# Kernel tuning notes

Measured on AMD Instinct MI355X. Metric: run time of the kernel, lower is better.

## Reference

```python
import jax, jax.numpy as jnp
import numpy as np
from jax import lax

B, GRID = 256, 58  # 28*2+2 per scn.InputLayer spatial size


def _conv(x, w):
    # x: [B,C,H,W], w: [O,C,k,k]; scn.Convolution is VALID, stride 1, no bias
    return lax.conv_general_dilated(
        x, w, window_strides=(1, 1), padding='VALID',
        dimension_numbers=('NCHW', 'OIHW', 'NCHW'))


def _maxpool2(x):
    return lax.reduce_window(x, -jnp.inf, lax.max,
                             window_dimensions=(1, 1, 2, 2),
                             window_strides=(1, 1, 2, 2), padding='VALID')


def setup_inputs() -> dict:
    key = jax.random.key(0)
    k0, k1, k2, k3, k4 = jax.random.split(key, 5)
    return {
        'x': jax.random.normal(k0, (B, 1, GRID, GRID), dtype=jnp.float32),
        'w1': jax.random.normal(k1, (64, 1, 5, 5), dtype=jnp.float32) * 0.1,
        'w2': jax.random.normal(k2, (128, 64, 5, 5), dtype=jnp.float32) * 0.025,
        'lw': jax.random.normal(k3, (10, 128), dtype=jnp.float32) * 0.09,
        'lb': jax.random.normal(k4, (10,), dtype=jnp.float32) * 0.01,
    }


def reference(x, w1, w2, lw, lb):
    h = _conv(x, w1)          # [B,64,54,54]
    h = _maxpool2(h)          # [B,64,27,27]
    h = _conv(h, w2)          # [B,128,23,23]
    h = jnp.transpose(h, (0, 2, 3, 1))  # channels-last for linear
    return jnp.einsum('bhwc,oc->bhwo', h, lw) + lb  # [B,23,23,10]
```

## Files before the change

kernel.cpp:

```cpp
#include <hip/hip_runtime.h>


typedef __attribute__((ext_vector_type(8))) short bf16x8;
typedef __attribute__((ext_vector_type(4))) float f32x4;
typedef __attribute__((ext_vector_type(16))) float f32x16;
typedef __attribute__((ext_vector_type(2))) unsigned int u32x2;
typedef __attribute__((ext_vector_type(4))) unsigned int u32x4;

#define MFMA16(a, b, c) __builtin_amdgcn_mfma_f32_16x16x32_bf16((a), (b), (c), 0, 0, 0)
#define MFMA32(a, b, c) __builtin_amdgcn_mfma_f32_32x32x16_bf16((a), (b), (c), 0, 0, 0)

static __device__ __forceinline__ unsigned short f2bf(float f) {
    unsigned u = __builtin_bit_cast(unsigned, f);
    u += 0x7FFFu + ((u >> 16) & 1u);
    return (unsigned short)(u >> 16);
}

__global__ __launch_bounds__(256) void prep_w2d(
    const float* __restrict__ w2, unsigned short* __restrict__ w2d)
{
    int t = blockIdx.x * 256 + threadIdx.x;
    if (t >= 25600) return;
    const int lane = t & 63, nt = (t >> 6) & 3, ks = (t >> 8) & 3, kk = t >> 10;
    const int oc = nt * 32 + (lane & 31);
    const int ic0 = ks * 16 + (lane >> 5) * 8;
    unsigned pk[4];
#pragma unroll
    for (int h = 0; h < 4; ++h) {
        unsigned short lo = f2bf(w2[oc * 1600 + (ic0 + 2 * h) * 25 + kk]);
        unsigned short hi = f2bf(w2[oc * 1600 + (ic0 + 2 * h + 1) * 25 + kk]);
        pk[h] = (unsigned)lo | ((unsigned)hi << 16);
    }
    u32x4 v; v.x = pk[0]; v.y = pk[1]; v.z = pk[2]; v.w = pk[3];
    *(u32x4*)(w2d + (size_t)t * 8) = v;
}

#define XS_STR   136
#define XBF_OFF  99144
#define W1T_OFF  105872
#define ECON_STR 272
#define LWT_OFF  147968
#define LDS_TOT  152320

__global__ __launch_bounds__(512, 2) void fused_net(
    const float* __restrict__ x, const float* __restrict__ w1,
    const unsigned short* __restrict__ w2d,
    const float* __restrict__ lw, const float* __restrict__ lb,
    float* __restrict__ out)
{
    extern __shared__ char lds[];
    unsigned short* xbf = (unsigned short*)(lds + XBF_OFF);
    unsigned short* w1t = (unsigned short*)(lds + W1T_OFF);
    const int b = blockIdx.x, tid = threadIdx.x;
    const int lane = tid & 63, w = tid >> 6;
    const int l16 = lane & 15, kg = lane >> 4;
    const int l32 = lane & 31, kg2 = lane >> 5;
    const int mgrp = w >> 1, ngrp = w & 1;

    const float4* xg = (const float4*)(x + b * 3364);
    for (int i = tid; i < 841; i += 512) {
        float4 v = xg[i];
        unsigned p0 = (unsigned)f2bf(v.x) | ((unsigned)f2bf(v.y) << 16);
        unsigned p1 = (unsigned)f2bf(v.z) | ((unsigned)f2bf(v.w) << 16);
        *(uint2*)(xbf + i * 4) = make_uint2(p0, p1);
    }
    for (int i = tid; i < 2048; i += 512) {
        int k = i >> 6, oc = i & 63;
        w1t[i] = (k < 25) ? f2bf(w1[oc * 25 + k]) : (unsigned short)0;
    }
    for (int i = tid; i < 2048; i += 512) {
        int o = i >> 7, cc = i & 127;
        float v = (o < 10) ? lw[o * 128 + cc] : 0.f;
        *(unsigned short*)(lds + LWT_OFF + o * 272 + cc * 2) = f2bf(v);
    }
    __syncthreads();

    {
        int koff[8];
        unsigned kmsk[8];
#pragma unroll
        for (int j = 0; j < 8; ++j) {
            int k = kg * 8 + j;
            int kh = k / 5, kw = k - 5 * kh;
            koff[j] = (k < 25) ? (kh * 58 + kw) : 0;
            kmsk[j] = (k < 25) ? 0xFFFFu : 0u;
        }
        bf16x8 bfrag[4];
#pragma unroll
        for (int ot = 0; ot < 4; ++ot)
#pragma unroll
            for (int j = 0; j < 8; ++j)
                bfrag[ot][j] = (short)w1t[(kg * 8 + j) * 64 + ot * 16 + l16];

        const f32x4 zero4 = {0.f, 0.f, 0.f, 0.f};
        for (int t = w; t < 183; t += 8) {
            int p = t * 4 + (l16 >> 2);
            if (p > 728) p = 728;
            const int q = l16 & 3;
            const int ph = p / 27, pw = p - 27 * ph;
            const int base = (2 * ph + (q >> 1)) * 58 + 2 * pw + (q & 1);
            bf16x8 afrag;
#pragma unroll
            for (int j = 0; j < 8; ++j)
                afrag[j] = (short)(xbf[base + koff[j]] & kmsk[j]);
            f32x4 acc1[4];
#pragma unroll
            for (int ot = 0; ot < 4; ++ot)
                acc1[ot] = MFMA16(afrag, bfrag[ot], zero4);
            const int pout = t * 4 + kg;
            if (pout < 729) {
#pragma unroll
                for (int ot = 0; ot < 4; ++ot) {
                    float m = fmaxf(fmaxf(acc1[ot][0], acc1[ot][1]),
                                    fmaxf(acc1[ot][2], acc1[ot][3]));
                    *(unsigned short*)(lds + pout * XS_STR + (ot * 16 + l16) * 2)
                        = f2bf(m);
                }
            }
        }
    }
    __syncthreads();

    const int mcnt = (mgrp == 0) ? 5 : 4;
    int ts[5], abase[5];
#pragma unroll
    for (int i = 0; i < 5; ++i) {
        int tile = (mgrp == 0) ? i : 5 + (mgrp - 1) * 4 + i;
        if (i >= mcnt) tile = mgrp;
        int tstart = tile * 32;
        if (tstart > 497) tstart = 497;
        ts[i] = tstart;
        const int sp = tstart + l32;
        const int oh = sp / 23, ow = sp - oh * 23;
        abase[i] = (oh * 27 + ow) * XS_STR + kg2 * 16;
    }

    f32x16 acc[5][2];
#pragma unroll
    for (int i = 0; i < 5; ++i)
#pragma unroll
        for (int j = 0; j < 2; ++j)
#pragma unroll
            for (int r = 0; r < 16; ++r) acc[i][j][r] = 0.f;

    for (int kk = 0; kk < 25; ++kk) {
        const int kh = kk / 5, kw = kk - 5 * kh;
        const int pixoff = (kh * 27 + kw) * XS_STR;
        bf16x8 Bf[4][2];
#pragma unroll
        for (int ks = 0; ks < 4; ++ks)
#pragma unroll
            for (int j = 0; j < 2; ++j)
                Bf[ks][j] = *(const bf16x8*)(
                    w2d + ((size_t)kk * 1024 + ks * 256 +
                           (ngrp * 2 + j) * 64 + lane) * 8);
#pragma unroll
        for (int ks = 0; ks < 4; ++ks) {
#pragma unroll
            for (int i = 0; i < 5; ++i) {
                if (i < mcnt) {
                    const char* ap = lds + abase[i] + pixoff + ks * 32;
                    u32x2 lo = *(const u32x2*)(ap);
                    u32x2 hi = *(const u32x2*)(ap + 8);
                    u32x4 t4; t4.x = lo.x; t4.y = lo.y; t4.z = hi.x; t4.w = hi.y;
                    bf16x8 a = __builtin_bit_cast(bf16x8, t4);
                    acc[i][0] = MFMA32(a, Bf[ks][0], acc[i][0]);
                    acc[i][1] = MFMA32(a, Bf[ks][1], acc[i][1]);
                }
            }
        }
    }

    __syncthreads();
#pragma unroll
    for (int i = 0; i < 5; ++i) {
        if (i < mcnt) {
#pragma unroll
            for (int j = 0; j < 2; ++j) {
                const int col = (ngrp * 2 + j) * 32 + l32;
#pragma unroll
                for (int reg = 0; reg < 16; ++reg) {
                    const int row = (reg & 3) + 8 * (reg >> 2) + 4 * kg2;
                    *(unsigned short*)(lds + (ts[i] + row) * ECON_STR + col * 2)
                        = f2bf(acc[i][j][reg]);
                }
            }
        }
    }
    __syncthreads();

    const float lbv = (l16 < 10) ? lb[l16] : 0.f;
#pragma unroll
    for (int i = 0; i < 5; ++i) {
        const int t = w + 8 * i;
        if (t < 34) {
            f32x4 al = {0.f, 0.f, 0.f, 0.f};
            const char* arow = lds + (t * 16 + l16) * ECON_STR + kg * 16;
            const char* brow = lds + LWT_OFF + l16 * 272 + kg * 16;
#pragma unroll
            for (int ks = 0; ks < 4; ++ks) {
                bf16x8 av = *(const bf16x8*)(arow + ks * 64);
                bf16x8 bv = *(const bf16x8*)(brow + ks * 64);
                al = MFMA16(av, bv, al);
            }
            if (l16 < 10) {
#pragma unroll
                for (int r = 0; r < 4; ++r) {
                    int sp = t * 16 + kg * 4 + r;
                    if (sp < 529)
                        out[((size_t)b * 529 + sp) * 10 + l16] = al[r] + lbv;
                }
            }
        }
    }
}

extern "C" void kernel_launch(void* const* d_in, const int* in_sizes, int n_in,
                              void* d_out, int out_size, void* d_ws, size_t ws_size,
                              hipStream_t stream) {
    const float* x  = (const float*)d_in[0];
    const float* w1 = (const float*)d_in[1];
    const float* w2 = (const float*)d_in[2];
    const float* lw = (const float*)d_in[3];
    const float* lb = (const float*)d_in[4];
    float* out = (float*)d_out;

    unsigned short* w2d = (unsigned short*)d_ws;

    (void)hipFuncSetAttribute((const void*)fused_net,
                              hipFuncAttributeMaxDynamicSharedMemorySize,
                              LDS_TOT);

    prep_w2d<<<100, 256, 0, stream>>>(w2, w2d);
    fused_net<<<256, 512, LDS_TOT, stream>>>(x, w1, w2d, lw, lb, out);
}
```

Baseline: 71.75 us.

## Split each image into two row halves per block to double grid parallelism

Each image is now handled by two blocks, each covering about half of the output rows. Each block computes conv1 and pooling only for the input rows its half needs, which cuts LDS to roughly half and raises launch bounds to 4 blocks per CU. The epilogue now stages each tile into a small per-wave-group buffer, and w2 fragments are loaded per k-step to lower register pressure. The cost is recomputing the overlapping halo rows of conv1 in both blocks and adding extra barriers in the epilogue.

```diff
diff --git a/kernel.cpp b/kernel.cpp
--- a/kernel.cpp
+++ b/kernel.cpp
@@ -36,13 +36,14 @@
 }
 
 #define XS_STR   136
-#define XBF_OFF  99144
-#define W1T_OFF  105872
+#define XBF_OFF  62424
+#define W1T_OFF  66832
+#define LWT_OFF  70928
 #define ECON_STR 272
-#define LWT_OFF  147968
-#define LDS_TOT  152320
-
-__global__ __launch_bounds__(512, 2) void fused_net(
+#define ECON_TILE 8704
+#define LDS_TOT  75280
+
+__global__ __launch_bounds__(512, 4) void fused_net(
     const float* __restrict__ x, const float* __restrict__ w1,
     const unsigned short* __restrict__ w2d,
     const float* __restrict__ lw, const float* __restrict__ lb,
@@ -51,18 +52,23 @@
     extern __shared__ char lds[];
     unsigned short* xbf = (unsigned short*)(lds + XBF_OFF);
     unsigned short* w1t = (unsigned short*)(lds + W1T_OFF);
-    const int b = blockIdx.x, tid = threadIdx.x;
+    const int h = blockIdx.x, b = blockIdx.y, tid = threadIdx.x;
     const int lane = tid & 63, w = tid >> 6;
     const int l16 = lane & 15, kg = lane >> 4;
     const int l32 = lane & 31, kg2 = lane >> 5;
     const int mgrp = w >> 1, ngrp = w & 1;
 
-    const float4* xg = (const float4*)(x + b * 3364);
-    for (int i = tid; i < 841; i += 512) {
-        float4 v = xg[i];
-        unsigned p0 = (unsigned)f2bf(v.x) | ((unsigned)f2bf(v.y) << 16);
-        unsigned p1 = (unsigned)f2bf(v.z) | ((unsigned)f2bf(v.w) << 16);
-        *(uint2*)(xbf + i * 4) = make_uint2(p0, p1);
+    const int ph0   = h ? 12 : 0;
+    const int x0    = h ? 24 : 0;
+    const int nxrow = h ? 34 : 38;
+    const int npx   = h ? 405 : 459;
+
+    const float* xb = x + b * 3364 + x0 * 58;
+    const int nf2 = nxrow * 29;
+    for (int i = tid; i < nf2; i += 512) {
+        float2 v = ((const float2*)xb)[i];
+        *(unsigned*)(xbf + i * 2) =
+            (unsigned)f2bf(v.x) | ((unsigned)f2bf(v.y) << 16);
     }
     for (int i = tid; i < 2048; i += 512) {
         int k = i >> 6, oc = i & 63;
@@ -71,7 +77,7 @@
     for (int i = tid; i < 2048; i += 512) {
         int o = i >> 7, cc = i & 127;
         float v = (o < 10) ? lw[o * 128 + cc] : 0.f;
-        *(unsigned short*)(lds + LWT_OFF + o * 272 + cc * 2) = f2bf(v);
+        *(unsigned short*)(lds + LWT_OFF + o * ECON_STR + cc * 2) = f2bf(v);
     }
     __syncthreads();
 
@@ -93,12 +99,14 @@
                 bfrag[ot][j] = (short)w1t[(kg * 8 + j) * 64 + ot * 16 + l16];
 
         const f32x4 zero4 = {0.f, 0.f, 0.f, 0.f};
-        for (int t = w; t < 183; t += 8) {
-            int p = t * 4 + (l16 >> 2);
-            if (p > 728) p = 728;
+        const int nt4 = (npx + 3) >> 2;
+        for (int t = w; t < nt4; t += 8) {
+            int pl = t * 4 + (l16 >> 2);
+            if (pl >= npx) pl = npx - 1;
             const int q = l16 & 3;
-            const int ph = p / 27, pw = p - 27 * ph;
-            const int base = (2 * ph + (q >> 1)) * 58 + 2 * pw + (q & 1);
+            const int pg = ph0 * 27 + pl;
+            const int ph = pg / 27, pw = pg - 27 * ph;
+            const int base = (2 * (ph - ph0) + (q >> 1)) * 58 + 2 * pw + (q & 1);
             bf16x8 afrag;
 #pragma unroll
             for (int j = 0; j < 8; ++j)
@@ -108,7 +116,7 @@
             for (int ot = 0; ot < 4; ++ot)
                 acc1[ot] = MFMA16(afrag, bfrag[ot], zero4);
             const int pout = t * 4 + kg;
-            if (pout < 729) {
+            if (pout < npx) {
 #pragma unroll
                 for (int ot = 0; ot < 4; ++ot) {
                     float m = fmaxf(fmaxf(acc1[ot][0], acc1[ot][1]),
@@ -121,23 +129,27 @@
     }
     __syncthreads();
 
-    const int mcnt = (mgrp == 0) ? 5 : 4;
-    int ts[5], abase[5];
-#pragma unroll
-    for (int i = 0; i < 5; ++i) {
-        int tile = (mgrp == 0) ? i : 5 + (mgrp - 1) * 4 + i;
-        if (i >= mcnt) tile = mgrp;
-        int tstart = tile * 32;
-        if (tstart > 497) tstart = 497;
-        ts[i] = tstart;
-        const int sp = tstart + l32;
+    int ts[3], mcnt;
+    if (h == 0) {
+        if (mgrp == 0) { mcnt = 3; ts[0] = 0; ts[1] = 32; ts[2] = 64; }
+        else { mcnt = 2; ts[0] = 96 + (mgrp - 1) * 64; ts[1] = ts[0] + 32;
+               ts[2] = ts[0]; }
+    } else {
+        mcnt = 2; ts[0] = 288 + mgrp * 64;
+        ts[1] = (mgrp == 3) ? 497 : ts[0] + 32;
+        ts[2] = ts[0];
+    }
+    int abase[3];
+#pragma unroll
+    for (int i = 0; i < 3; ++i) {
+        const int sp = ts[i] + l32;
         const int oh = sp / 23, ow = sp - oh * 23;
-        abase[i] = (oh * 27 + ow) * XS_STR + kg2 * 16;
-    }
-
-    f32x16 acc[5][2];
-#pragma unroll
-    for (int i = 0; i < 5; ++i)
+        abase[i] = ((oh - ph0) * 27 + ow) * XS_STR + kg2 * 16;
+    }
+
+    f32x16 acc[3][2];
+#pragma unroll
+    for (int i = 0; i < 3; ++i)
 #pragma unroll
         for (int j = 0; j < 2; ++j)
 #pragma unroll
@@ -146,73 +158,69 @@
     for (int kk = 0; kk < 25; ++kk) {
         const int kh = kk / 5, kw = kk - 5 * kh;
         const int pixoff = (kh * 27 + kw) * XS_STR;
-        bf16x8 Bf[4][2];
-#pragma unroll
-        for (int ks = 0; ks < 4; ++ks)
-#pragma unroll
-            for (int j = 0; j < 2; ++j)
-                Bf[ks][j] = *(const bf16x8*)(
-                    w2d + ((size_t)kk * 1024 + ks * 256 +
-                           (ngrp * 2 + j) * 64 + lane) * 8);
+        const unsigned short* wp = w2d + ((size_t)kk * 1024 + lane) * 8;
 #pragma unroll
         for (int ks = 0; ks < 4; ++ks) {
-#pragma unroll
-            for (int i = 0; i < 5; ++i) {
+            const bf16x8 B0 = *(const bf16x8*)(wp + (ks * 256 + (ngrp*2+0)*64) * 8);
+            const bf16x8 B1 = *(const bf16x8*)(wp + (ks * 256 + (ngrp*2+1)*64) * 8);
+#pragma unroll
+            for (int i = 0; i < 3; ++i) {
                 if (i < mcnt) {
                     const char* ap = lds + abase[i] + pixoff + ks * 32;
                     u32x2 lo = *(const u32x2*)(ap);
                     u32x2 hi = *(const u32x2*)(ap + 8);
                     u32x4 t4; t4.x = lo.x; t4.y = lo.y; t4.z = hi.x; t4.w = hi.y;
                     bf16x8 a = __builtin_bit_cast(bf16x8, t4);
-                    acc[i][0] = MFMA32(a, Bf[ks][0], acc[i][0]);
-                    acc[i][1] = MFMA32(a, Bf[ks][1], acc[i][1]);
+                    acc[i][0] = MFMA32(a, B0, acc[i][0]);
+                    acc[i][1] = MFMA32(a, B1, acc[i][1]);
                 }
             }
         }
     }
 
-    __syncthreads();
-#pragma unroll
-    for (int i = 0; i < 5; ++i) {
-        if (i < mcnt) {
-#pragma unroll
-            for (int j = 0; j < 2; ++j) {
-                const int col = (ngrp * 2 + j) * 32 + l32;
-#pragma unroll
-                for (int reg = 0; reg < 16; ++reg) {
-                    const int row = (reg & 3) + 8 * (reg >> 2) + 4 * kg2;
-                    *(unsigned short*)(lds + (ts[i] + row) * ECON_STR + col * 2)
-                        = f2bf(acc[i][j][reg]);
-                }
-            }
-        }
-    }
-    __syncthreads();
-
+    char* myecon = lds + mgrp * ECON_TILE;
     const float lbv = (l16 < 10) ? lb[l16] : 0.f;
-#pragma unroll
-    for (int i = 0; i < 5; ++i) {
-        const int t = w + 8 * i;
-        if (t < 34) {
-            f32x4 al = {0.f, 0.f, 0.f, 0.f};
-            const char* arow = lds + (t * 16 + l16) * ECON_STR + kg * 16;
-            const char* brow = lds + LWT_OFF + l16 * 272 + kg * 16;
-#pragma unroll
-            for (int ks = 0; ks < 4; ++ks) {
-                bf16x8 av = *(const bf16x8*)(arow + ks * 64);
-                bf16x8 bv = *(const bf16x8*)(brow + ks * 64);
-                al = MFMA16(av, bv, al);
-            }
-            if (l16 < 10) {
-#pragma unroll
-                for (int r = 0; r < 4; ++r) {
-                    int sp = t * 16 + kg * 4 + r;
-                    if (sp < 529)
-                        out[((size_t)b * 529 + sp) * 10 + l16] = al[r] + lbv;
-                }
-            }
-        }
-    }
+
+#define EPI(IT)                                                               \
+    {                                                                         \
+        __syncthreads();                                                      \
+        if ((IT) < mcnt) {                                                    \
+            _Pragma("unroll")                                                 \
+            for (int j = 0; j < 2; ++j) {                                     \
+                const int col = (ngrp * 2 + j) * 32 + l32;                    \
+                _Pragma("unroll")                                             \
+                for (int reg = 0; reg < 16; ++reg) {                          \
+                    const int row = (reg & 3) + 8 * (reg >> 2) + 4 * kg2;     \
+                    *(unsigned short*)(myecon + row * ECON_STR + col * 2)     \
+                        = f2bf(acc[(IT)][j][reg]);                            \
+                }                                                             \
+            }                                                                 \
+        }                                                                     \
+        __syncthreads();                                                      \
+        if ((IT) < mcnt) {                                                    \
+            f32x4 al = {0.f, 0.f, 0.f, 0.f};                                  \
+            const char* arow = myecon + (ngrp * 16 + l16) * ECON_STR + kg * 16;\
+            const char* brow = lds + LWT_OFF + l16 * ECON_STR + kg * 16;      \
+            _Pragma("unroll")                                                 \
+            for (int ks = 0; ks < 4; ++ks) {                                  \
+                bf16x8 av = *(const bf16x8*)(arow + ks * 64);                 \
+                bf16x8 bv = *(const bf16x8*)(brow + ks * 64);                 \
+                al = MFMA16(av, bv, al);                                      \
+            }                                                                 \
+            if (l16 < 10) {                                                   \
+                _Pragma("unroll")                                             \
+                for (int r = 0; r < 4; ++r) {                                 \
+                    const int sp = ts[(IT)] + ngrp * 16 + kg * 4 + r;         \
+                    out[((size_t)b * 529 + sp) * 10 + l16] = al[r] + lbv;     \
+                }                                                             \
+            }                                                                 \
+        }                                                                     \
+    }
+
+    EPI(0);
+    EPI(1);
+    if (h == 0) { EPI(2); }
+#undef EPI
 }
 
 extern "C" void kernel_launch(void* const* d_in, const int* in_sizes, int n_in,
@@ -232,5 +240,5 @@
                               LDS_TOT);
 
     prep_w2d<<<100, 256, 0, stream>>>(w2, w2d);
-    fused_net<<<256, 512, LDS_TOT, stream>>>(x, w1, w2d, lw, lb, out);
-}
+    fused_net<<<dim3(2, 256), 512, LDS_TOT, stream>>>(x, w1, w2d, lw, lb, out);
+}
```

New measurement: 80.14 us. 1.12x slower.
